# Optimization experiments

Measured on AMD Instinct MI355X. Metric: run time of the kernel, lower is better.

Reference implementation:

```python
import jax, jax.numpy as jnp
import numpy as np

NODE_DIM = 256
EDGE_DIM = 64
TIME_DIM = 1024
HEADS = 8
HEAD_DIM = NODE_DIM // HEADS
MLP = 2
BS, N = 32, 48
BN = BS * N
E = BS * N * (N - 1)


def _lin(k, fin, fout):
    return jax.random.normal(k, (fin, fout), dtype=jnp.float32) / np.sqrt(fin)


def _edge_index():
    idx = np.arange(N)
    src, dst = np.meshgrid(idx, idx, indexing='ij')
    m = src != dst
    src, dst = src[m], dst[m]              # [N*(N-1)] per graph
    offs = (np.arange(BS) * N)[:, None]
    row = (offs + src[None, :]).reshape(-1)
    col = (offs + dst[None, :]).reshape(-1)
    return jnp.asarray(np.stack([row, col]), dtype=jnp.int32)


def setup_inputs() -> dict:
    key = jax.random.key(0)
    ks = jax.random.split(key, 32)
    d = {
        'pos': jax.random.normal(ks[0], (BN, 3), jnp.float32),
        'h': jax.random.normal(ks[1], (BN, NODE_DIM), jnp.float32),
        'edge_attr': jax.random.normal(ks[2], (E, EDGE_DIM), jnp.float32),
        'node_mask': jnp.ones((BN, 1), jnp.float32),
        'node_time_emb': jax.random.normal(ks[3], (BN, TIME_DIM), jnp.float32),
        'edge_time_emb': jax.random.normal(ks[4], (E, TIME_DIM), jnp.float32),
        'edge_index': _edge_index(),
        # edge_emb: Linear(edge_dim+1 -> edge_dim)
        'W_ee': _lin(ks[5], EDGE_DIM + 1, EDGE_DIM), 'b_ee': jnp.zeros((EDGE_DIM,)),
        # AdaLN time MLPs (SiLU -> Linear)
        'W_nt': _lin(ks[6], TIME_DIM, 6 * NODE_DIM), 'b_nt': jnp.zeros((6 * NODE_DIM,)),
        'W_et': _lin(ks[7], TIME_DIM, 6 * EDGE_DIM), 'b_et': jnp.zeros((6 * EDGE_DIM,)),
        # Trans_Layer sparse attention
        'Wq': _lin(ks[8], NODE_DIM, NODE_DIM), 'bq': jnp.zeros((NODE_DIM,)),
        'Wk': _lin(ks[9], NODE_DIM, NODE_DIM), 'bk': jnp.zeros((NODE_DIM,)),
        'Wv': _lin(ks[10], NODE_DIM, NODE_DIM), 'bv': jnp.zeros((NODE_DIM,)),
        'We0': _lin(ks[11], EDGE_DIM, NODE_DIM),
        'We1': _lin(ks[12], EDGE_DIM, NODE_DIM),
        'W_n2e': _lin(ks[13], NODE_DIM, EDGE_DIM), 'b_n2e': jnp.zeros((EDGE_DIM,)),
        # node FFN
        'W_ff1': _lin(ks[14], NODE_DIM, MLP * NODE_DIM), 'b_ff1': jnp.zeros((MLP * NODE_DIM,)),
        'W_ff2': _lin(ks[15], MLP * NODE_DIM, NODE_DIM), 'b_ff2': jnp.zeros((NODE_DIM,)),
        # edge FFN
        'W_ff3': _lin(ks[16], EDGE_DIM, MLP * EDGE_DIM), 'b_ff3': jnp.zeros((MLP * EDGE_DIM,)),
        'W_ff4': _lin(ks[17], MLP * EDGE_DIM, EDGE_DIM), 'b_ff4': jnp.zeros((EDGE_DIM,)),
        # CondEquiUpdate
        'coors_scale': jnp.full((1,), 0.01, jnp.float32),
        'W_ut': _lin(ks[18], TIME_DIM, 2 * NODE_DIM), 'b_ut': jnp.zeros((2 * NODE_DIM,)),
        'W_ui': _lin(ks[19], 2 * NODE_DIM + EDGE_DIM + 1, NODE_DIM), 'b_ui': jnp.zeros((NODE_DIM,)),
        'W_uc1': _lin(ks[20], NODE_DIM, NODE_DIM), 'b_uc1': jnp.zeros((NODE_DIM,)),
        'W_uc2': _lin(ks[21], NODE_DIM, 1),
    }
    return d


def _ln(x):  # LayerNorm, no affine, eps=1e-6
    m = x.mean(-1, keepdims=True)
    v = ((x - m) ** 2).mean(-1, keepdims=True)
    return (x - m) * jax.lax.rsqrt(v + 1e-6)


def _modulate(x, shift, scale):
    return x * (1 + scale) + shift


def _block(pos, h, edge_attr, node_mask, node_time_emb, edge_time_emb, edge_index,
           W_ee, b_ee, W_nt, b_nt, W_et, b_et, Wq, bq, Wk, bk, Wv, bv, We0, We1,
           W_n2e, b_n2e, W_ff1, b_ff1, W_ff2, b_ff2, W_ff3, b_ff3, W_ff4, b_ff4,
           coors_scale, W_ut, b_ut, W_ui, b_ui, W_uc1, b_uc1, W_uc2):
    row, col = edge_index[0], edge_index[1]  # row = source j, col = target i
    diff = pos[row] - pos[col]                              # [E,3]
    dist = jnp.sqrt(jnp.sum(diff * diff, -1, keepdims=True) + 1e-12)  # [E,1]
    ea = jnp.concatenate([dist, edge_attr], -1) @ W_ee + b_ee

    nt = jax.nn.silu(node_time_emb) @ W_nt + b_nt
    n_sh_msa, n_sc_msa, n_g_msa, n_sh_mlp, n_sc_mlp, n_g_mlp = jnp.split(nt, 6, axis=1)
    et = jax.nn.silu(edge_time_emb) @ W_et + b_et
    e_sh_msa, e_sc_msa, e_g_msa, e_sh_mlp, e_sc_mlp, e_g_mlp = jnp.split(et, 6, axis=1)

    hh = _modulate(_ln(h), n_sh_msa, n_sc_msa)
    ea = _modulate(_ln(ea), e_sh_msa, e_sc_msa)

    # sparse multi-head attention over edges (Trans_Layer)
    q = (hh @ Wq + bq).reshape(BN, HEADS, HEAD_DIM)
    k = (hh @ Wk + bk).reshape(BN, HEADS, HEAD_DIM)
    v = (hh @ Wv + bv).reshape(BN, HEADS, HEAD_DIM)
    e0 = (ea @ We0).reshape(E, HEADS, HEAD_DIM)
    e1 = (ea @ We1).reshape(E, HEADS, HEAD_DIM)
    alpha = jnp.sum(q[col] * k[row] * e0, -1) / np.sqrt(HEAD_DIM)  # [E,H]
    mx = jax.ops.segment_max(alpha, col, num_segments=BN)
    ex = jnp.exp(alpha - mx[col])
    den = jax.ops.segment_sum(ex, col, num_segments=BN)
    att = ex / (den[col] + 1e-16)
    msg = v[row] * e1 * att[:, :, None]
    h_node = jax.ops.segment_sum(msg, col, num_segments=BN).reshape(BN, NODE_DIM)

    h_edge = (h_node[row] + h_node[col]) @ W_n2e + b_n2e

    h_node = h + n_g_msa * h_node
    h_node = _modulate(_ln(h_node), n_sh_mlp, n_sc_mlp) * node_mask
    ff = jax.nn.silu(h_node @ W_ff1 + b_ff1) @ W_ff2 + b_ff2
    h_out = (h_node + n_g_mlp * ff) * node_mask

    h_e = edge_attr + e_g_msa * h_edge
    h_e = _modulate(_ln(h_e), e_sh_mlp, e_sc_mlp)
    ffe = jax.nn.silu(h_e @ W_ff3 + b_ff3) @ W_ff4 + b_ff4
    h_edge_out = h_e + e_g_mlp * ffe

    # CondEquiUpdate: equivariant coordinate update
    h_input = jnp.concatenate([h_out[row], h_out[col], h_edge_out, dist], -1)
    nrm = jnp.linalg.norm(diff, axis=-1, keepdims=True)
    cdiff = diff / jnp.clip(nrm, 1e-8) * coors_scale        # CoorsNorm(scale_init=0.01)
    t_shift, t_scale = jnp.split(jax.nn.silu(edge_time_emb) @ W_ut + b_ut, 2, axis=1)
    inv = _modulate(_ln(h_input @ W_ui + b_ui), t_shift, t_scale)
    inv = jnp.tanh(jax.nn.silu(inv @ W_uc1 + b_uc1) @ W_uc2)  # [E,1]
    trans = cdiff * inv
    pos_out = pos + jax.ops.segment_sum(trans, row, num_segments=BN)
    return h_out, h_edge_out, pos_out


def reference(pos, h, edge_attr, node_mask, node_time_emb, edge_time_emb, edge_index,
              W_ee, b_ee, W_nt, b_nt, W_et, b_et, Wq, bq, Wk, bk, Wv, bv, We0, We1,
              W_n2e, b_n2e, W_ff1, b_ff1, W_ff2, b_ff2, W_ff3, b_ff3, W_ff4, b_ff4,
              coors_scale, W_ut, b_ut, W_ui, b_ui, W_uc1, b_uc1, W_uc2):
    return _block(pos, h, edge_attr, node_mask, node_time_emb, edge_time_emb, edge_index,
                  W_ee, b_ee, W_nt, b_nt, W_et, b_et, Wq, bq, Wk, bk, Wv, bv, We0, We1,
                  W_n2e, b_n2e, W_ff1, b_ff1, W_ff2, b_ff2, W_ff3, b_ff3, W_ff4, b_ff4,
                  coors_scale, W_ut, b_ut, W_ui, b_ui, W_uc1, b_uc1, W_uc2)
```

## Files before the change

### kernel.cpp

```cpp
#include <hip/hip_runtime.h>

typedef unsigned short u16;
typedef __attribute__((ext_vector_type(4))) u16 u16x4;
typedef __attribute__((ext_vector_type(8))) u16 u16x8;
typedef __attribute__((ext_vector_type(8))) short s16x8;
typedef __attribute__((ext_vector_type(4))) float f32x4;

#define E_CNT 72192
#define BN_CNT 1536
#define EPG 2256

__device__ __forceinline__ float b2f(u16 u) {
    union { unsigned int i; float f; } x; x.i = ((unsigned int)u) << 16; return x.f;
}
__device__ __forceinline__ u16 f2b(float f) {
    union { float f; unsigned int i; } x; x.f = f;
    unsigned int r = x.i + 0x7fffu + ((x.i >> 16) & 1u);
    return (u16)(r >> 16);
}
__device__ __forceinline__ float siluf(float x) { return x / (1.f + expf(-x)); }

__device__ __forceinline__ void gll16(const void* g, void* l) {
    __builtin_amdgcn_global_load_lds(
        (const __attribute__((address_space(1))) void*)g,
        (__attribute__((address_space(3))) void*)l, 16, 0, 0);
}

__device__ __forceinline__ float wave_ln64(float x) {
    float s = x;
    #pragma unroll
    for (int off = 1; off < 64; off <<= 1) s += __shfl_xor(s, off);
    float mean = s * 0.015625f;
    float d = x - mean;
    float v2 = d * d;
    #pragma unroll
    for (int off = 1; off < 64; off <<= 1) v2 += __shfl_xor(v2, off);
    return d * rsqrtf(v2 * 0.015625f + 1e-6f);
}

__device__ __forceinline__ float block_ln256(float x) {
    __shared__ float tmp[4];
    int t = threadIdx.x;
    float s = x;
    #pragma unroll
    for (int off = 1; off < 64; off <<= 1) s += __shfl_xor(s, off);
    if ((t & 63) == 0) tmp[t >> 6] = s;
    __syncthreads();
    float mean = (tmp[0] + tmp[1] + tmp[2] + tmp[3]) * (1.f / 256.f);
    float d = x - mean;
    float v2 = d * d;
    #pragma unroll
    for (int off = 1; off < 64; off <<= 1) v2 += __shfl_xor(v2, off);
    __syncthreads();
    if ((t & 63) == 0) tmp[t >> 6] = v2;
    __syncthreads();
    float var = (tmp[0] + tmp[1] + tmp[2] + tmp[3]) * (1.f / 256.f);
    return d * rsqrtf(var + 1e-6f);
}

template<int ACT, int OUTBF>
__global__ __launch_bounds__(256) void k_gemm(
    const u16* __restrict__ A, const u16* __restrict__ Bt,
    const float* __restrict__ bias, void* __restrict__ C,
    int M, int N, int K)
{
    __shared__ u16 As[64][40];
    __shared__ u16 Bs[64][40];
    int bn0 = blockIdx.x * 64, bm0 = blockIdx.y * 64;
    int t = threadIdx.x;
    int lane = t & 63, wave = t >> 6;
    int wm = wave >> 1, wn = wave & 1;
    int lr = t >> 2, lc = (t & 3) * 8;
    f32x4 acc[2][2] = {};
    const u16* Ap = A + (size_t)(bm0 + lr) * K + lc;
    const u16* Bp = Bt + (size_t)(bn0 + lr) * K + lc;
    int fr = lane & 15, fk = (lane >> 4) * 8;
    for (int k0 = 0; k0 < K; k0 += 32) {
        *(u16x8*)&As[lr][lc] = *(const u16x8*)(Ap + k0);
        *(u16x8*)&Bs[lr][lc] = *(const u16x8*)(Bp + k0);
        __syncthreads();
        s16x8 a0 = *(const s16x8*)&As[wm * 32 + fr][fk];
        s16x8 a1 = *(const s16x8*)&As[wm * 32 + 16 + fr][fk];
        s16x8 b0 = *(const s16x8*)&Bs[wn * 32 + fr][fk];
        s16x8 b1 = *(const s16x8*)&Bs[wn * 32 + 16 + fr][fk];
        acc[0][0] = __builtin_amdgcn_mfma_f32_16x16x32_bf16(a0, b0, acc[0][0], 0, 0, 0);
        acc[0][1] = __builtin_amdgcn_mfma_f32_16x16x32_bf16(a0, b1, acc[0][1], 0, 0, 0);
        acc[1][0] = __builtin_amdgcn_mfma_f32_16x16x32_bf16(a1, b0, acc[1][0], 0, 0, 0);
        acc[1][1] = __builtin_amdgcn_mfma_f32_16x16x32_bf16(a1, b1, acc[1][1], 0, 0, 0);
        __syncthreads();
    }
    int cIn = lane & 15, r4 = (lane >> 4) * 4;
    #pragma unroll
    for (int i = 0; i < 2; i++)
    #pragma unroll
    for (int j = 0; j < 2; j++) {
        int col = bn0 + wn * 32 + j * 16 + cIn;
        float bv = bias ? bias[col] : 0.f;
        #pragma unroll
        for (int r = 0; r < 4; r++) {
            int rowg = bm0 + wm * 32 + i * 16 + r4 + r;
            float vv = acc[i][j][r] + bv;
            if (ACT == 1) vv = siluf(vv);
            if (OUTBF) ((u16*)C)[(size_t)rowg * N + col] = f2b(vv);
            else       ((float*)C)[(size_t)rowg * N + col] = vv;
        }
    }
}

template<int ACT, int OUTBF>
__global__ __launch_bounds__(256) void k_gemm128(
    const u16* __restrict__ A, const u16* __restrict__ Bt,
    const float* __restrict__ bias, void* __restrict__ C,
    int M, int N, int K)
{
    __shared__ u16 As[128 * 32];
    __shared__ u16 Bs[128 * 32];
    const int t = threadIdx.x;
    const int lane = t & 63, wv = t >> 6;
    const int wm = wv >> 1, wn = wv & 1;
    const int nwg = gridDim.x * gridDim.y;
    const int orig = blockIdx.y * gridDim.x + blockIdx.x;
    const int q8 = nwg >> 3, r8 = nwg & 7;
    const int xcd = orig & 7, lin = orig >> 3;
    const int wgid = (xcd < r8 ? xcd * (q8 + 1) : r8 * (q8 + 1) + (xcd - r8) * q8) + lin;
    const int bxs = wgid % gridDim.x, bys = wgid / gridDim.x;
    const int bn0 = bxs * 128, bm0 = bys * 128;
    const int srow = t >> 2, scol = (t & 3) * 8;
    const u16* Ap = A + (size_t)(bm0 + srow) * K + scol;
    const u16* Bp = Bt + (size_t)(bn0 + srow) * K + scol;
    const size_t rstep = (size_t)64 * K;
    u16* AsW = As + (size_t)(wv * 16) * 32;
    u16* BsW = Bs + (size_t)(wv * 16) * 32;
    const int fr = lane & 15, fk = (lane >> 4) * 8;
    const u16* aBase = As + (size_t)(wm * 64) * 32;
    const u16* bBase = Bs + (size_t)(wn * 64) * 32;
    f32x4 acc[4][4] = {};
    for (int k0 = 0; k0 < K; k0 += 32) {
        gll16(Ap + k0, AsW);
        gll16(Ap + k0 + rstep, AsW + 64 * 32);
        gll16(Bp + k0, BsW);
        gll16(Bp + k0 + rstep, BsW + 64 * 32);
        __syncthreads();
        s16x8 af[4], bfr[4];
        #pragma unroll
        for (int m = 0; m < 4; m++) af[m] = *(const s16x8*)&aBase[(size_t)(m * 16 + fr) * 32 + fk];
        #pragma unroll
        for (int n = 0; n < 4; n++) bfr[n] = *(const s16x8*)&bBase[(size_t)(n * 16 + fr) * 32 + fk];
        #pragma unroll
        for (int m = 0; m < 4; m++)
        #pragma unroll
        for (int n = 0; n < 4; n++)
            acc[m][n] = __builtin_amdgcn_mfma_f32_16x16x32_bf16(af[m], bfr[n], acc[m][n], 0, 0, 0);
        __syncthreads();
    }
    const int cIn = lane & 15, r4 = (lane >> 4) * 4;
    #pragma unroll
    for (int n = 0; n < 4; n++) {
        int col = bn0 + wn * 64 + n * 16 + cIn;
        float bv = bias ? bias[col] : 0.f;
        #pragma unroll
        for (int m = 0; m < 4; m++) {
            #pragma unroll
            for (int r = 0; r < 4; r++) {
                int rowg = bm0 + wm * 64 + m * 16 + r4 + r;
                float vv = acc[m][n][r] + bv;
                if (ACT == 1) vv = siluf(vv);
                if (OUTBF) ((u16*)C)[(size_t)rowg * N + col] = f2b(vv);
                else       ((float*)C)[(size_t)rowg * N + col] = vv;
            }
        }
    }
}

struct ConvJob { const float* W; u16* Wt; int ldw, k0, n0, K, nc_start; };
struct CopyJob { const float* src; float* dst; int n; };
struct BatchArgs { ConvJob cj[17]; CopyJob cp[5]; int conv_blocks; };

__global__ __launch_bounds__(256) void k_prep(BatchArgs a)
{
    int b = blockIdx.x;
    if (b < a.conv_blocks) {
        int j = 0;
        #pragma unroll 1
        while (j + 1 < 17 && a.cj[j + 1].nc_start <= b) ++j;
        const ConvJob J = a.cj[j];
        int n = b - J.nc_start;
        for (int k = threadIdx.x; k < J.K; k += 256)
            J.Wt[(size_t)n * J.K + k] = f2b(J.W[(size_t)(J.k0 + k) * J.ldw + J.n0 + n]);
    } else {
        int c = b - a.conv_blocks;
        const CopyJob C = a.cp[c];
        for (int i = threadIdx.x; i < C.n; i += 256) C.dst[i] = C.src[i];
    }
}

__global__ void k_silu_bf(const float* __restrict__ in, u16* __restrict__ out, int n4)
{
    int i = blockIdx.x * 256 + threadIdx.x;
    int stride = gridDim.x * 256;
    for (; i < n4; i += stride) {
        f32x4 v = *(const f32x4*)(in + (size_t)i * 4);
        u16x4 o;
        #pragma unroll
        for (int j = 0; j < 4; j++) o[j] = f2b(siluf(v[j]));
        *(u16x4*)(out + (size_t)i * 4) = o;
    }
}

__global__ __launch_bounds__(256) void k_edge_pre(
    const float* __restrict__ pos, const float* __restrict__ edge_attr,
    const int* __restrict__ ei, const float* __restrict__ W_ee,
    const float* __restrict__ b_ee, const float* __restrict__ coors_scale,
    const u16* __restrict__ etf,
    u16* __restrict__ ea_mod, float* __restrict__ dist, float* __restrict__ cdiff)
{
    __shared__ float Ws[65][64];
    int t = threadIdx.x;
    for (int i = t; i < 65 * 64; i += 256) Ws[i >> 6][i & 63] = W_ee[i];
    __syncthreads();
    int l = t & 63;
    float bee = b_ee[l];
    float cscale = coors_scale[0];
    for (int g = 0; g < 16; g++) {
        int e = blockIdx.x * 64 + g * 4 + (t >> 6);
        int row = ei[e], col = ei[E_CNT + e];
        float d0 = pos[row * 3 + 0] - pos[col * 3 + 0];
        float d1 = pos[row * 3 + 1] - pos[col * 3 + 1];
        float d2 = pos[row * 3 + 2] - pos[col * 3 + 2];
        float ssq = d0 * d0 + d1 * d1 + d2 * d2;
        float dst = sqrtf(ssq + 1e-12f);
        float nrm = sqrtf(ssq);
        float cs = cscale / fmaxf(nrm, 1e-8f);
        if (l == 0) {
            dist[e] = dst;
            cdiff[e * 3 + 0] = d0 * cs; cdiff[e * 3 + 1] = d1 * cs; cdiff[e * 3 + 2] = d2 * cs;
        }
        float attr = edge_attr[(size_t)e * 64 + l];
        float acc = dst * Ws[0][l];
        for (int f = 0; f < 64; f++) acc += __shfl(attr, f) * Ws[1 + f][l];
        acc += bee;
        float y = wave_ln64(acc);
        const u16* ep = etf + (size_t)e * 896;
        float m = y * (1.f + b2f(ep[64 + l])) + b2f(ep[l]);
        ea_mod[(size_t)e * 64 + l] = f2b(m);
    }
}

__global__ __launch_bounds__(256) void k_node_hh(
    const float* __restrict__ h, const float* __restrict__ nt, u16* __restrict__ hh)
{
    int n = blockIdx.x, c = threadIdx.x;
    float x = h[(size_t)n * 256 + c];
    float y = block_ln256(x);
    float m = y * (1.f + nt[(size_t)n * 1536 + 256 + c]) + nt[(size_t)n * 1536 + c];
    hh[(size_t)n * 256 + c] = f2b(m);
}

__global__ __launch_bounds__(256) void k_agg(
    const float* __restrict__ qkv, const u16* __restrict__ e01,
    float* __restrict__ hnode, u16* __restrict__ hnode_bf)
{
    int n = blockIdx.x;
    int b = n / 48, i = n % 48;
    int t = threadIdx.x;
    __shared__ float qs[8][33];
    __shared__ float att[47][8];
    __shared__ float mxs[8], dens[8];
    __shared__ int elist[47], slist[47];
    qs[t >> 5][t & 31] = qkv[(size_t)n * 768 + t];
    if (t < 47) {
        int s = t + (t >= i ? 1 : 0);
        slist[t] = s;
        elist[t] = b * EPG + s * 47 + (i < s ? i : i - 1);
    }
    __syncthreads();
    for (int idx = t; idx < 376; idx += 256) {
        int j = idx >> 3, hh = idx & 7;
        int src = b * 48 + slist[j];
        int e = elist[j];
        const float* kp = qkv + (size_t)src * 768 + 256 + hh * 32;
        const u16* ep = e01 + (size_t)e * 512 + hh * 32;
        float p = 0.f;
        #pragma unroll
        for (int d = 0; d < 32; d++) p += qs[hh][d] * kp[d] * b2f(ep[d]);
        att[j][hh] = p * 0.17677669529663687f;
    }
    __syncthreads();
    if (t < 8) {
        float m = -1e30f;
        for (int j = 0; j < 47; j++) m = fmaxf(m, att[j][t]);
        float den = 0.f;
        for (int j = 0; j < 47; j++) den += expf(att[j][t] - m);
        mxs[t] = m; dens[t] = den + 1e-16f;
    }
    __syncthreads();
    for (int idx = t; idx < 376; idx += 256) {
        int j = idx >> 3, hh = idx & 7;
        att[j][hh] = expf(att[j][hh] - mxs[hh]) / dens[hh];
    }
    __syncthreads();
    int c = t, hh = t >> 5;
    float acc = 0.f;
    for (int j = 0; j < 47; j++) {
        int src = b * 48 + slist[j];
        int e = elist[j];
        acc += att[j][hh] * qkv[(size_t)src * 768 + 512 + c] * b2f(e01[(size_t)e * 512 + 256 + c]);
    }
    hnode[(size_t)n * 256 + c] = acc;
    hnode_bf[(size_t)n * 256 + c] = f2b(acc);
}

__global__ __launch_bounds__(256) void k_node_mod(
    const float* __restrict__ h, const float* __restrict__ hnode_raw,
    const float* __restrict__ nt, const float* __restrict__ mask,
    float* __restrict__ hmod, u16* __restrict__ hmod_bf)
{
    int n = blockIdx.x, c = threadIdx.x;
    float x = h[(size_t)n * 256 + c] + nt[(size_t)n * 1536 + 512 + c] * hnode_raw[(size_t)n * 256 + c];
    float y = block_ln256(x);
    float m = (y * (1.f + nt[(size_t)n * 1536 + 1024 + c]) + nt[(size_t)n * 1536 + 768 + c]) * mask[n];
    hmod[(size_t)n * 256 + c] = m;
    hmod_bf[(size_t)n * 256 + c] = f2b(m);
}

__global__ void k_hout(const float* __restrict__ hmod, const float* __restrict__ ff2,
                       const float* __restrict__ nt, const float* __restrict__ mask,
                       float* __restrict__ out, u16* __restrict__ hout_bf)
{
    int i = blockIdx.x * 256 + threadIdx.x;
    if (i >= BN_CNT * 256) return;
    int n = i >> 8, c = i & 255;
    float v = (hmod[i] + nt[(size_t)n * 1536 + 1280 + c] * ff2[i]) * mask[n];
    out[i] = v;
    hout_bf[i] = f2b(v);
}

__global__ __launch_bounds__(256) void k_edge_mod(
    const float* __restrict__ Q1, const float* __restrict__ b_n2e,
    const float* __restrict__ edge_attr, const int* __restrict__ ei,
    const u16* __restrict__ etf, float* __restrict__ hemod, u16* __restrict__ hemod_bf)
{
    int e = blockIdx.x * 4 + (threadIdx.x >> 6);
    int l = threadIdx.x & 63;
    int row = ei[e], col = ei[E_CNT + e];
    float hedge = Q1[(size_t)row * 64 + l] + Q1[(size_t)col * 64 + l] + b_n2e[l];
    const u16* ep = etf + (size_t)e * 896;
    float x = edge_attr[(size_t)e * 64 + l] + b2f(ep[128 + l]) * hedge;
    float y = wave_ln64(x);
    float m = y * (1.f + b2f(ep[256 + l])) + b2f(ep[192 + l]);
    hemod[(size_t)e * 64 + l] = m;
    hemod_bf[(size_t)e * 64 + l] = f2b(m);
}

__global__ void k_edge_out(const float* __restrict__ hemod, const float* __restrict__ ff4,
                           const u16* __restrict__ etf,
                           float* __restrict__ out2, u16* __restrict__ heout_bf)
{
    size_t i = (size_t)blockIdx.x * 256 + threadIdx.x;
    if (i >= (size_t)E_CNT * 64) return;
    int e = (int)(i >> 6), c = (int)(i & 63);
    float v = hemod[i] + b2f(etf[(size_t)e * 896 + 320 + c]) * ff4[i];
    out2[i] = v;
    heout_bf[i] = f2b(v);
}

__global__ __launch_bounds__(256) void k_inv_pre(
    const float* __restrict__ p12,
    const u16* __restrict__ P3, const float* __restrict__ dist,
    const float* __restrict__ W_ui, const float* __restrict__ b_ui,
    const int* __restrict__ ei, const u16* __restrict__ etf, u16* __restrict__ invmod)
{
    int e = blockIdx.x, c = threadIdx.x;
    int row = ei[e], col = ei[E_CNT + e];
    float x = p12[(size_t)row * 512 + c] + p12[(size_t)col * 512 + 256 + c]
            + b2f(P3[(size_t)e * 256 + c]) + dist[e] * W_ui[576 * 256 + c] + b_ui[c];
    float y = block_ln256(x);
    const u16* ep = etf + (size_t)e * 896;
    float m = y * (1.f + b2f(ep[640 + c])) + b2f(ep[384 + c]);
    invmod[(size_t)e * 256 + c] = f2b(m);
}

__global__ __launch_bounds__(256) void k_inv(const u16* __restrict__ uc1,
                                             const float* __restrict__ W_uc2,
                                             float* __restrict__ inv)
{
    int e = blockIdx.x * 4 + (threadIdx.x >> 6);
    int l = threadIdx.x & 63;
    u16x4 v = *(const u16x4*)(uc1 + (size_t)e * 256 + l * 4);
    const float* w = W_uc2 + l * 4;
    float s = b2f(v[0]) * w[0] + b2f(v[1]) * w[1] + b2f(v[2]) * w[2] + b2f(v[3]) * w[3];
    #pragma unroll
    for (int off = 1; off < 64; off <<= 1) s += __shfl_xor(s, off);
    if (l == 0) inv[e] = tanhf(s);
}

__global__ void k_pos(const float* __restrict__ pos, const float* __restrict__ cdiff,
                      const float* __restrict__ inv, float* __restrict__ out3)
{
    int n = blockIdx.x * 256 + threadIdx.x;
    if (n >= BN_CNT) return;
    int b = n / 48, s = n % 48;
    int e0 = b * EPG + s * 47;
    float a0 = 0.f, a1 = 0.f, a2 = 0.f;
    for (int j = 0; j < 47; j++) {
        float f = inv[e0 + j];
        a0 += cdiff[(size_t)(e0 + j) * 3 + 0] * f;
        a1 += cdiff[(size_t)(e0 + j) * 3 + 1] * f;
        a2 += cdiff[(size_t)(e0 + j) * 3 + 2] * f;
    }
    out3[n * 3 + 0] = pos[n * 3 + 0] + a0;
    out3[n * 3 + 1] = pos[n * 3 + 1] + a1;
    out3[n * 3 + 2] = pos[n * 3 + 2] + a2;
}

extern "C" void kernel_launch(void* const* d_in, const int* in_sizes, int n_in,
                              void* d_out, int out_size, void* d_ws, size_t ws_size,
                              hipStream_t stream)
{
    (void)in_sizes; (void)n_in; (void)out_size; (void)ws_size;
    const float* pos       = (const float*)d_in[0];
    const float* h         = (const float*)d_in[1];
    const float* edge_attr = (const float*)d_in[2];
    const float* node_mask = (const float*)d_in[3];
    const float* nte       = (const float*)d_in[4];
    const float* ete       = (const float*)d_in[5];
    const int*   ei        = (const int*)d_in[6];
    const float* W_ee = (const float*)d_in[7];  const float* b_ee = (const float*)d_in[8];
    const float* W_nt = (const float*)d_in[9];  const float* b_nt = (const float*)d_in[10];
    const float* W_et = (const float*)d_in[11]; const float* b_et = (const float*)d_in[12];
    const float* Wq  = (const float*)d_in[13];  const float* bq  = (const float*)d_in[14];
    const float* Wk  = (const float*)d_in[15];  const float* bk  = (const float*)d_in[16];
    const float* Wv  = (const float*)d_in[17];  const float* bv  = (const float*)d_in[18];
    const float* We0 = (const float*)d_in[19];  const float* We1 = (const float*)d_in[20];
    const float* W_n2e = (const float*)d_in[21]; const float* b_n2e = (const float*)d_in[22];
    const float* W_ff1 = (const float*)d_in[23]; const float* b_ff1 = (const float*)d_in[24];
    const float* W_ff2 = (const float*)d_in[25]; const float* b_ff2 = (const float*)d_in[26];
    const float* W_ff3 = (const float*)d_in[27]; const float* b_ff3 = (const float*)d_in[28];
    const float* W_ff4 = (const float*)d_in[29]; const float* b_ff4 = (const float*)d_in[30];
    const float* coors_scale = (const float*)d_in[31];
    const float* W_ut = (const float*)d_in[32]; const float* b_ut = (const float*)d_in[33];
    const float* W_ui = (const float*)d_in[34]; const float* b_ui = (const float*)d_in[35];
    const float* W_uc1 = (const float*)d_in[36]; const float* b_uc1 = (const float*)d_in[37];
    const float* W_uc2 = (const float*)d_in[38];

    const size_t E = E_CNT;
    char* ws = (char*)d_ws;
    size_t off = 0;
    auto AL = [&](size_t b) { size_t o = off; off += (b + 255) & ~(size_t)255; return o; };

    size_t o_wtcat  = AL(896 * 1024 * 2);
    size_t o_wtnt   = AL(1536 * 1024 * 2);
    size_t o_wtqkv  = AL(768 * 256 * 2);
    size_t o_wte01  = AL(512 * 64 * 2);
    size_t o_wtn2e  = AL(64 * 256 * 2);
    size_t o_wtff1  = AL(512 * 256 * 2), o_wtff2 = AL(256 * 512 * 2);
    size_t o_wtff3  = AL(128 * 64 * 2),  o_wtff4 = AL(64 * 128 * 2);
    size_t o_wtuiab = AL(512 * 256 * 2);
    size_t o_wtuic  = AL(256 * 64 * 2),  o_wtuc1 = AL(256 * 256 * 2);
    size_t o_bias896 = AL(896 * 4);
    size_t o_bias768 = AL(768 * 4);
    size_t o_reg1 = AL(E * 1024 * 2);
    size_t o_etf  = AL(E * 896 * 2);
    size_t o_ntes = AL(1536 * 1024 * 2);
    size_t o_ntf  = AL((size_t)1536 * 1536 * 4);
    size_t o_eamod = AL(E * 64 * 2);
    size_t o_dist = AL(E * 4), o_cdiff = AL(E * 12);
    size_t o_qkv  = AL(1536 * 768 * 4);
    size_t o_reg3 = AL(E * 512 * 2);
    size_t o_hnode = AL(1536 * 256 * 4), o_hnodebf = AL(1536 * 256 * 2);
    size_t o_q1 = AL(1536 * 64 * 4);
    size_t o_hh = AL(1536 * 256 * 2);
    size_t o_hmod = AL(1536 * 256 * 4), o_hmodbf = AL(1536 * 256 * 2);
    size_t o_ff1 = AL(1536 * 512 * 2), o_ff2 = AL(1536 * 256 * 4);
    size_t o_houtbf = AL(1536 * 256 * 2);
    size_t o_hemod = AL(E * 64 * 4), o_hemodbf = AL(E * 64 * 2);
    size_t o_p12 = AL(1536 * 512 * 4);
    size_t o_inv = AL(E * 4);
    size_t o_etes = o_reg1;
    size_t o_p3 = o_reg1;
    size_t o_invmod = o_reg1 + E * 256 * 2;
    size_t o_uc1o = o_reg1 + E * 256 * 4;
    size_t o_e01 = o_reg3;
    size_t o_ffem = o_reg3;
    size_t o_ff4o = o_reg3 + E * 128 * 2;
    size_t o_heoutbf = o_reg3 + E * 128 * 2 + E * 64 * 4;

    #define WSU(o) ((u16*)(ws + (o)))
    #define WSF(o) ((float*)(ws + (o)))

    {
        BatchArgs a;
        int s = 0; int j = 0;
        auto add = [&](const float* W, u16* Wt, int ldw, int k0, int n0, int K, int NC) {
            a.cj[j++] = ConvJob{W, Wt, ldw, k0, n0, K, s}; s += NC;
        };
        add(W_et, WSU(o_wtcat), 384, 0, 0, 1024, 384);
        add(W_ut, WSU(o_wtcat) + (size_t)384 * 1024, 512, 0, 0, 1024, 512);
        add(W_nt, WSU(o_wtnt), 1536, 0, 0, 1024, 1536);
        add(Wq, WSU(o_wtqkv), 256, 0, 0, 256, 256);
        add(Wk, WSU(o_wtqkv) + (size_t)256 * 256, 256, 0, 0, 256, 256);
        add(Wv, WSU(o_wtqkv) + (size_t)512 * 256, 256, 0, 0, 256, 256);
        add(We0, WSU(o_wte01), 256, 0, 0, 64, 256);
        add(We1, WSU(o_wte01) + (size_t)256 * 64, 256, 0, 0, 64, 256);
        add(W_n2e, WSU(o_wtn2e), 64, 0, 0, 256, 64);
        add(W_ff1, WSU(o_wtff1), 512, 0, 0, 256, 512);
        add(W_ff2, WSU(o_wtff2), 256, 0, 0, 512, 256);
        add(W_ff3, WSU(o_wtff3), 128, 0, 0, 64, 128);
        add(W_ff4, WSU(o_wtff4), 64, 0, 0, 128, 64);
        add(W_ui, WSU(o_wtuiab), 256, 0, 0, 256, 256);
        add(W_ui, WSU(o_wtuiab) + (size_t)256 * 256, 256, 256, 0, 256, 256);
        add(W_ui, WSU(o_wtuic), 256, 512, 0, 64, 256);
        add(W_uc1, WSU(o_wtuc1), 256, 0, 0, 256, 256);
        a.conv_blocks = s;
        a.cp[0] = CopyJob{b_et, WSF(o_bias896), 384};
        a.cp[1] = CopyJob{b_ut, WSF(o_bias896) + 384, 512};
        a.cp[2] = CopyJob{bq, WSF(o_bias768), 256};
        a.cp[3] = CopyJob{bk, WSF(o_bias768) + 256, 256};
        a.cp[4] = CopyJob{bv, WSF(o_bias768) + 512, 256};
        k_prep<<<s + 5, 256, 0, stream>>>(a);
    }

    k_silu_bf<<<2048, 256, 0, stream>>>(ete, WSU(o_etes), (int)(E * 1024 / 4));
    k_silu_bf<<<1024, 256, 0, stream>>>(nte, WSU(o_ntes), 1536 * 1024 / 4);

    k_gemm128<0, 1><<<dim3(7, 564), 256, 0, stream>>>(WSU(o_etes), WSU(o_wtcat), WSF(o_bias896), WSU(o_etf), E_CNT, 896, 1024);
    k_gemm<0, 0><<<dim3(24, 24), 256, 0, stream>>>(WSU(o_ntes), WSU(o_wtnt), b_nt, WSF(o_ntf), 1536, 1536, 1024);

    k_edge_pre<<<1128, 256, 0, stream>>>(pos, edge_attr, ei, W_ee, b_ee, coors_scale,
                                         WSU(o_etf), WSU(o_eamod), WSF(o_dist), WSF(o_cdiff));

    k_node_hh<<<1536, 256, 0, stream>>>(h, WSF(o_ntf), WSU(o_hh));
    k_gemm<0, 0><<<dim3(12, 24), 256, 0, stream>>>(WSU(o_hh), WSU(o_wtqkv), WSF(o_bias768), WSF(o_qkv), 1536, 768, 256);
    k_gemm128<0, 1><<<dim3(4, 564), 256, 0, stream>>>(WSU(o_eamod), WSU(o_wte01), nullptr, WSU(o_e01), E_CNT, 512, 64);
    k_agg<<<1536, 256, 0, stream>>>(WSF(o_qkv), WSU(o_e01), WSF(o_hnode), WSU(o_hnodebf));

    k_gemm<0, 0><<<dim3(1, 24), 256, 0, stream>>>(WSU(o_hnodebf), WSU(o_wtn2e), nullptr, WSF(o_q1), 1536, 64, 256);

    k_node_mod<<<1536, 256, 0, stream>>>(h, WSF(o_hnode), WSF(o_ntf), node_mask, WSF(o_hmod), WSU(o_hmodbf));
    k_gemm<1, 1><<<dim3(8, 24), 256, 0, stream>>>(WSU(o_hmodbf), WSU(o_wtff1), b_ff1, WSU(o_ff1), 1536, 512, 256);
    k_gemm<0, 0><<<dim3(4, 24), 256, 0, stream>>>(WSU(o_ff1), WSU(o_wtff2), b_ff2, WSF(o_ff2), 1536, 256, 512);
    k_hout<<<1536, 256, 0, stream>>>(WSF(o_hmod), WSF(o_ff2), WSF(o_ntf), node_mask, (float*)d_out, WSU(o_houtbf));

    k_edge_mod<<<18048, 256, 0, stream>>>(WSF(o_q1), b_n2e, edge_attr, ei, WSU(o_etf), WSF(o_hemod), WSU(o_hemodbf));
    k_gemm128<1, 1><<<dim3(1, 564), 256, 0, stream>>>(WSU(o_hemodbf), WSU(o_wtff3), b_ff3, WSU(o_ffem), E_CNT, 128, 64);
    k_gemm<0, 0><<<dim3(1, 1128), 256, 0, stream>>>(WSU(o_ffem), WSU(o_wtff4), b_ff4, WSF(o_ff4o), E_CNT, 64, 128);
    k_edge_out<<<18048, 256, 0, stream>>>(WSF(o_hemod), WSF(o_ff4o), WSU(o_etf),
                                          (float*)d_out + 393216, WSU(o_heoutbf));

    k_gemm<0, 0><<<dim3(8, 24), 256, 0, stream>>>(WSU(o_houtbf), WSU(o_wtuiab), nullptr, WSF(o_p12), 1536, 512, 256);
    k_gemm128<0, 1><<<dim3(2, 564), 256, 0, stream>>>(WSU(o_heoutbf), WSU(o_wtuic), nullptr, WSU(o_p3), E_CNT, 256, 64);
    k_inv_pre<<<E_CNT, 256, 0, stream>>>(WSF(o_p12), WSU(o_p3), WSF(o_dist),
                                         W_ui, b_ui, ei, WSU(o_etf), WSU(o_invmod));
    k_gemm128<1, 1><<<dim3(2, 564), 256, 0, stream>>>(WSU(o_invmod), WSU(o_wtuc1), b_uc1, WSU(o_uc1o), E_CNT, 256, 256);
    k_inv<<<18048, 256, 0, stream>>>(WSU(o_uc1o), W_uc2, WSF(o_inv));
    k_pos<<<6, 256, 0, stream>>>(pos, WSF(o_cdiff), WSF(o_inv), (float*)d_out + 393216 + E_CNT * 64);

    #undef WSU
    #undef WSF
}
```

Measured before the change: 777.4 us.

## Double-buffer LDS in 128x128 GEMM to overlap global loads with MFMA

```diff
diff --git a/kernel.cpp b/kernel.cpp
--- a/kernel.cpp
+++ b/kernel.cpp
@@ -113,8 +113,8 @@
     const float* __restrict__ bias, void* __restrict__ C,
     int M, int N, int K)
 {
-    __shared__ u16 As[128 * 32];
-    __shared__ u16 Bs[128 * 32];
+    __shared__ u16 As[2][128 * 32];
+    __shared__ u16 Bs[2][128 * 32];
     const int t = threadIdx.x;
     const int lane = t & 63, wv = t >> 6;
     const int wm = wv >> 1, wn = wv & 1;
@@ -129,30 +129,49 @@
     const u16* Ap = A + (size_t)(bm0 + srow) * K + scol;
     const u16* Bp = Bt + (size_t)(bn0 + srow) * K + scol;
     const size_t rstep = (size_t)64 * K;
-    u16* AsW = As + (size_t)(wv * 16) * 32;
-    u16* BsW = Bs + (size_t)(wv * 16) * 32;
+    const int woff = wv * 16 * 32;
     const int fr = lane & 15, fk = (lane >> 4) * 8;
-    const u16* aBase = As + (size_t)(wm * 64) * 32;
-    const u16* bBase = Bs + (size_t)(wn * 64) * 32;
     f32x4 acc[4][4] = {};
-    for (int k0 = 0; k0 < K; k0 += 32) {
-        gll16(Ap + k0, AsW);
-        gll16(Ap + k0 + rstep, AsW + 64 * 32);
-        gll16(Bp + k0, BsW);
-        gll16(Bp + k0 + rstep, BsW + 64 * 32);
-        __syncthreads();
+
+    auto STAGE = [&](int b, int ko) {
+        gll16(Ap + ko, &As[b][woff]);
+        gll16(Ap + ko + rstep, &As[b][woff + 64 * 32]);
+        gll16(Bp + ko, &Bs[b][woff]);
+        gll16(Bp + ko + rstep, &Bs[b][woff + 64 * 32]);
+    };
+    auto COMPUTE = [&](int b) {
+        const u16* aBase = &As[b][wm * 64 * 32];
+        const u16* bBase = &Bs[b][wn * 64 * 32];
         s16x8 af[4], bfr[4];
         #pragma unroll
-        for (int m = 0; m < 4; m++) af[m] = *(const s16x8*)&aBase[(size_t)(m * 16 + fr) * 32 + fk];
-        #pragma unroll
-        for (int n = 0; n < 4; n++) bfr[n] = *(const s16x8*)&bBase[(size_t)(n * 16 + fr) * 32 + fk];
+        for (int m = 0; m < 4; m++) af[m] = *(const s16x8*)&aBase[(m * 16 + fr) * 32 + fk];
+        #pragma unroll
+        for (int n = 0; n < 4; n++) bfr[n] = *(const s16x8*)&bBase[(n * 16 + fr) * 32 + fk];
         #pragma unroll
         for (int m = 0; m < 4; m++)
         #pragma unroll
         for (int n = 0; n < 4; n++)
             acc[m][n] = __builtin_amdgcn_mfma_f32_16x16x32_bf16(af[m], bfr[n], acc[m][n], 0, 0, 0);
-        __syncthreads();
-    }
+    };
+
+    STAGE(0, 0);
+    int cur = 0;
+    for (int k0 = 0; k0 < K - 32; k0 += 32) {
+        STAGE(cur ^ 1, k0 + 32);
+        __builtin_amdgcn_sched_barrier(0);
+        asm volatile("s_waitcnt vmcnt(4)" ::: "memory");
+        __builtin_amdgcn_sched_barrier(0);
+        __builtin_amdgcn_s_barrier();
+        COMPUTE(cur);
+        __builtin_amdgcn_s_barrier();
+        __builtin_amdgcn_sched_barrier(0);
+        cur ^= 1;
+    }
+    asm volatile("s_waitcnt vmcnt(0)" ::: "memory");
+    __builtin_amdgcn_sched_barrier(0);
+    __builtin_amdgcn_s_barrier();
+    COMPUTE(cur);
+
     const int cIn = lane & 15, r4 = (lane >> 4) * 4;
     #pragma unroll
     for (int n = 0; n < 4; n++) {
```

Measured after the change: 758.9 us. -2.4%, faster.
